# Optimization experiments

Measured on AMD Instinct MI355X. Metric: run time of the kernel, lower is better.

## Reference

```python
import jax, jax.numpy as jnp
import numpy as np

D_MODEL = 1024
D_STATE = 16
D_CONV = 4
EXPAND = 2
D_INNER = D_MODEL * EXPAND
B_SZ, L_SEQ = 4, 1024


def setup_inputs() -> dict:
    key = jax.random.key(0)
    ks = jax.random.split(key, 8)
    s = lambda fan_in: 1.0 / np.sqrt(fan_in)
    x = jax.random.normal(ks[0], (B_SZ, L_SEQ, D_MODEL), dtype=jnp.float32)
    in_proj_w = jax.random.uniform(ks[1], (2 * D_INNER, D_MODEL), jnp.float32, -s(D_MODEL), s(D_MODEL))
    conv_w = jax.random.uniform(ks[2], (D_INNER, 1, D_CONV), jnp.float32, -s(D_CONV), s(D_CONV))
    conv_b = jax.random.uniform(ks[3], (D_INNER,), jnp.float32, -s(D_CONV), s(D_CONV))
    x_proj_w = jax.random.uniform(ks[4], (2 * D_STATE + D_INNER, D_INNER), jnp.float32, -s(D_INNER), s(D_INNER))
    dt_proj_w = jax.random.uniform(ks[5], (D_INNER, D_INNER), jnp.float32, -s(D_INNER), s(D_INNER))
    dt_proj_b = jax.random.uniform(ks[6], (D_INNER,), jnp.float32, -1e-3, 1e-3)
    A = jnp.tile(jnp.arange(1, D_STATE + 1, dtype=jnp.float32), (D_INNER, 1))
    A_log = jnp.log(A)
    D_param = jnp.ones((D_INNER,), jnp.float32)
    out_proj_w = jax.random.uniform(ks[7], (D_MODEL, D_INNER), jnp.float32, -s(D_INNER), s(D_INNER))
    return {"x": x, "in_proj_w": in_proj_w, "conv_w": conv_w, "conv_b": conv_b,
            "x_proj_w": x_proj_w, "dt_proj_w": dt_proj_w, "dt_proj_b": dt_proj_b,
            "A_log": A_log, "D_param": D_param, "out_proj_w": out_proj_w}


def _selective_scan(x, delta, Bp, Cp, A_log, D_param):
    # x, delta: [B, L, D]; Bp, Cp: [B, L, N]
    A = -jnp.exp(A_log)                                   # [D, N]
    deltaA = jnp.exp(delta[..., None] * A)                # [B, L, D, N]
    deltaB_x = delta[..., None] * Bp[:, :, None, :] * x[..., None]  # [B, L, D, N]

    def step(h, inp):
        dA, dBx, Ct = inp                                 # [B,D,N], [B,D,N], [B,N]
        h = dA * h + dBx
        y = jnp.einsum('bn,bdn->bd', Ct, h)
        return h, y

    h0 = jnp.zeros((x.shape[0], x.shape[2], A.shape[1]), x.dtype)
    xs = (jnp.swapaxes(deltaA, 0, 1), jnp.swapaxes(deltaB_x, 0, 1), jnp.swapaxes(Cp, 0, 1))
    _, ys = jax.lax.scan(step, h0, xs)                    # ys: [L, B, D]
    return jnp.swapaxes(ys, 0, 1) + x * D_param


def reference(x, in_proj_w, conv_w, conv_b, x_proj_w, dt_proj_w, dt_proj_b, A_log, D_param, out_proj_w):
    B, L, _ = x.shape
    xz = x @ in_proj_w.T                                  # [B, L, 2*D_inner]
    xi, z = jnp.split(xz, 2, axis=-1)
    # causal depthwise conv (pad left K-1 == pad both & truncate to L)
    xc = jnp.swapaxes(xi, 1, 2)                           # [B, D_inner, L]
    xc = jax.lax.conv_general_dilated(xc, conv_w, window_strides=(1,),
                                      padding=[(D_CONV - 1, 0)],
                                      feature_group_count=D_INNER,
                                      dimension_numbers=('NCH', 'OIH', 'NCH'))
    xc = xc + conv_b[None, :, None]
    xi = jax.nn.silu(jnp.swapaxes(xc, 1, 2))              # [B, L, D_inner]
    deltaBC = xi @ x_proj_w.T
    delta, Bp, Cp = jnp.split(deltaBC, [D_INNER, D_INNER + D_STATE], axis=-1)
    delta = jax.nn.softplus(delta @ dt_proj_w.T + dt_proj_b)
    y = _selective_scan(xi, delta, Bp, Cp, A_log, D_param)
    return (y * jax.nn.silu(z)) @ out_proj_w.T
```

## Files before the change

### kernel.cpp

```cpp
#include <hip/hip_runtime.h>
#include <math.h>

#define B_SZ 4
#define L_SEQ 1024
#define D_MODEL 1024
#define D_INNER 2048
#define D_STATE 16
#define N_BC 2080
#define M_ROWS (B_SZ * L_SEQ)
#define CHUNK 32
#define NCH (L_SEQ / CHUNK)

typedef unsigned short u16;
typedef __bf16 bf16x8 __attribute__((ext_vector_type(8)));
typedef float f32x4 __attribute__((ext_vector_type(4)));

typedef const __attribute__((address_space(1))) unsigned short glb_u16;
typedef __attribute__((address_space(3))) unsigned short lds_u16;

__device__ __forceinline__ void gload_lds16(const u16* g, u16* l) {
    __builtin_amdgcn_global_load_lds((glb_u16*)g, (lds_u16*)l, 16, 0, 0);
}

__device__ __forceinline__ float bf2f(u16 u) {
    union { unsigned int i; float f; } v; v.i = ((unsigned int)u) << 16; return v.f;
}
__device__ __forceinline__ u16 f2bf(float f) {
    union { float f; unsigned int i; } v; v.f = f;
    return (u16)((v.i + 0x7FFFu + ((v.i >> 16) & 1u)) >> 16);
}
__device__ __forceinline__ float softplus_f(float v) {
    return fmaxf(v, 0.f) + log1pf(expf(-fabsf(v)));
}
__device__ __forceinline__ float silu_f(float v) {
    return v / (1.f + expf(-v));
}

__global__ __launch_bounds__(256) void cvt_bf16_k(const float* __restrict__ in,
                                                  u16* __restrict__ out, int n4) {
    int i = blockIdx.x * 256 + threadIdx.x;
    if (i >= n4) return;
    float4 v = *(const float4*)(in + (size_t)i * 4);
    ushort4 o;
    o.x = f2bf(v.x); o.y = f2bf(v.y); o.z = f2bf(v.z); o.w = f2bf(v.w);
    *(ushort4*)(out + (size_t)i * 4) = o;
}

template <int EPI>
__global__ __launch_bounds__(256, 2) void gemm_bf16(
    const u16* __restrict__ A, int lda,
    const u16* __restrict__ W, int ldw,
    int M, int N, int K, int ldc,
    const float* __restrict__ bias,
    float* __restrict__ Cf, u16* __restrict__ Cb, float* __restrict__ Caux)
{
    __shared__ __align__(16) u16 As[128 * 32];
    __shared__ __align__(16) u16 Ws[128 * 32];

    const int tid = threadIdx.x;
    const int lane = tid & 63;
    const int wave = tid >> 6;
    const int wr = wave >> 1;
    const int wc = wave & 1;
    const int bm = blockIdx.y * 128;
    const int bn = blockIdx.x * 128;
    const int l15 = lane & 15;
    const int lq = lane >> 4;

    const int lrow = lane >> 2;
    const int qoff = (((lane & 3) ^ ((lane >> 3) & 3))) * 8;
    const int rq = ((lq ^ ((l15 >> 1) & 3))) * 8;

    f32x4 acc[4][4];
#pragma unroll
    for (int m = 0; m < 4; ++m)
#pragma unroll
        for (int n = 0; n < 4; ++n) acc[m][n] = f32x4{0.f, 0.f, 0.f, 0.f};

    for (int k0 = 0; k0 < K; k0 += 32) {
#pragma unroll
        for (int i = 0; i < 2; ++i) {
            const int c = wave * 2 + i;
            const int row = c * 16 + lrow;
            gload_lds16(A + (size_t)(bm + row) * lda + k0 + qoff, &As[c * 512]);
            int wrow = bn + row; if (wrow >= N) wrow = N - 1;
            gload_lds16(W + (size_t)wrow * ldw + k0 + qoff, &Ws[c * 512]);
        }
        __syncthreads();

        bf16x8 af[4], bfr[4];
#pragma unroll
        for (int m = 0; m < 4; ++m) {
            int r = wr * 64 + m * 16 + l15;
            af[m] = *reinterpret_cast<const bf16x8*>(&As[r * 32 + rq]);
        }
#pragma unroll
        for (int n = 0; n < 4; ++n) {
            int r = wc * 64 + n * 16 + l15;
            bfr[n] = *reinterpret_cast<const bf16x8*>(&Ws[r * 32 + rq]);
        }
#pragma unroll
        for (int m = 0; m < 4; ++m)
#pragma unroll
            for (int n = 0; n < 4; ++n)
                acc[m][n] = __builtin_amdgcn_mfma_f32_16x16x32_bf16(af[m], bfr[n], acc[m][n], 0, 0, 0);
        __syncthreads();
    }

#pragma unroll
    for (int m = 0; m < 4; ++m) {
#pragma unroll
        for (int n = 0; n < 4; ++n) {
#pragma unroll
            for (int j = 0; j < 4; ++j) {
                int gr = bm + wr * 64 + m * 16 + lq * 4 + j;
                int gc = bn + wc * 64 + n * 16 + l15;
                float v = acc[m][n][j];
                if (EPI == 0) {
                    if (gc < N) Cf[(size_t)gr * ldc + gc] = v;
                } else if (EPI == 1) {
                    if (gc < N) Cf[(size_t)gr * ldc + gc] = softplus_f(v + bias[gc]);
                } else if (EPI == 2) {
                    if (gc < N) Cb[(size_t)gr * ldc + gc] = f2bf(v);
                } else {
                    if (gc < D_INNER) Cb[(size_t)gr * D_INNER + gc] = f2bf(v);
                    else if (gc < N_BC) Caux[(size_t)gr * 32 + (gc - D_INNER)] = v;
                }
            }
        }
    }
}

__global__ __launch_bounds__(256) void conv_silu_k(
    const u16* __restrict__ xz,
    const float* __restrict__ cw,
    const float* __restrict__ cb,
    u16* __restrict__ xc)
{
    int idx = blockIdx.x * 256 + threadIdx.x;
    if (idx >= M_ROWS * D_INNER) return;
    int d = idx & (D_INNER - 1);
    int m = idx >> 11;
    int l = m & (L_SEQ - 1);
    float4 w = *(const float4*)(cw + d * 4);
    const u16* base = xz + (size_t)m * (2 * D_INNER) + d;
    float acc = cb[d];
    acc = fmaf(bf2f(base[0]), w.w, acc);
    if (l >= 1) acc = fmaf(bf2f(base[-(2 * D_INNER)]), w.z, acc);
    if (l >= 2) acc = fmaf(bf2f(base[-2 * (2 * D_INNER)]), w.y, acc);
    if (l >= 3) acc = fmaf(bf2f(base[-3 * (2 * D_INNER)]), w.x, acc);
    xc[idx] = f2bf(silu_f(acc));
}

__global__ __launch_bounds__(256) void scan_pass1(
    const float* __restrict__ delta,
    const u16* __restrict__ xc,
    const float* __restrict__ BC,
    const float* __restrict__ A_log,
    float* __restrict__ hbuf,
    float* __restrict__ sumd)
{
    __shared__ float Bs[CHUNK][16];
    const int bid = blockIdx.x;
    const int c = bid & (NCH - 1);
    const int dblk = (bid >> 5) & 7;
    const int b = bid >> 8;
    const int tid = threadIdx.x;
    const int d = dblk * 256 + tid;
    const int row0 = b * L_SEQ + c * CHUNK;

    if (tid < CHUNK * 16) {
        int l = tid >> 4, n = tid & 15;
        Bs[l][n] = BC[(size_t)(row0 + l) * 32 + n];
    }
    __syncthreads();

    float Ac[16], h[16];
#pragma unroll
    for (int n = 0; n < 16; ++n) { Ac[n] = -__expf(A_log[d * 16 + n]); h[n] = 0.f; }
    float sd = 0.f;

    for (int l = 0; l < CHUNK; ++l) {
        size_t r = (size_t)(row0 + l);
        float dv = delta[r * D_INNER + d];
        float xv = bf2f(xc[r * D_INNER + d]);
        float t = dv * xv;
        sd += dv;
#pragma unroll
        for (int n = 0; n < 16; ++n) {
            float dA = __expf(dv * Ac[n]);
            h[n] = fmaf(dA, h[n], t * Bs[l][n]);
        }
    }
    size_t base = ((size_t)(b * NCH + c) * 16) * D_INNER + d;
#pragma unroll
    for (int n = 0; n < 16; ++n) hbuf[base + (size_t)n * D_INNER] = h[n];
    sumd[(size_t)(b * NCH + c) * D_INNER + d] = sd;
}

__global__ __launch_bounds__(256) void scan_pass2(
    const float* __restrict__ A_log,
    const float* __restrict__ sumd,
    float* __restrict__ hbuf)
{
    const int bid = blockIdx.x;
    const int dblk = bid & 7;
    const int n = (bid >> 3) & 15;
    const int b = bid >> 7;
    const int d = dblk * 256 + threadIdx.x;
    const float Ac = -__expf(A_log[d * 16 + n]);
    float carry = 0.f;
    for (int c = 0; c < NCH; ++c) {
        float sd = sumd[(size_t)(b * NCH + c) * D_INNER + d];
        size_t idx = ((size_t)(b * NCH + c) * 16 + n) * D_INNER + d;
        float tmp = hbuf[idx];
        hbuf[idx] = carry;
        carry = fmaf(__expf(Ac * sd), carry, tmp);
    }
}

__global__ __launch_bounds__(256) void scan_pass3(
    const float* __restrict__ delta,
    const u16* __restrict__ xc,
    const float* __restrict__ BC,
    const u16* __restrict__ xz,
    const float* __restrict__ A_log,
    const float* __restrict__ Dp,
    const float* __restrict__ hbuf,
    u16* __restrict__ yg)
{
    __shared__ float BCs[CHUNK][32];
    const int bid = blockIdx.x;
    const int c = bid & (NCH - 1);
    const int dblk = (bid >> 5) & 7;
    const int b = bid >> 8;
    const int tid = threadIdx.x;
    const int d = dblk * 256 + tid;
    const int row0 = b * L_SEQ + c * CHUNK;

#pragma unroll
    for (int i = 0; i < (CHUNK * 32) / 256; ++i) {
        int e = tid + i * 256;
        int l = e >> 5, j = e & 31;
        BCs[l][j] = BC[(size_t)(row0 + l) * 32 + j];
    }
    __syncthreads();

    float Ac[16], h[16];
    size_t base = ((size_t)(b * NCH + c) * 16) * D_INNER + d;
#pragma unroll
    for (int n = 0; n < 16; ++n) {
        Ac[n] = -__expf(A_log[d * 16 + n]);
        h[n] = hbuf[base + (size_t)n * D_INNER];
    }
    const float Dv = Dp[d];

    for (int l = 0; l < CHUNK; ++l) {
        size_t r = (size_t)(row0 + l);
        float dv = delta[r * D_INNER + d];
        float xv = bf2f(xc[r * D_INNER + d]);
        float t = dv * xv;
        float y = xv * Dv;
#pragma unroll
        for (int n = 0; n < 16; ++n) {
            float dA = __expf(dv * Ac[n]);
            h[n] = fmaf(dA, h[n], t * BCs[l][n]);
            y = fmaf(BCs[l][16 + n], h[n], y);
        }
        float zv = bf2f(xz[r * (2 * D_INNER) + D_INNER + d]);
        yg[r * D_INNER + d] = f2bf(y * silu_f(zv));
    }
}

extern "C" void kernel_launch(void* const* d_in, const int* in_sizes, int n_in,
                              void* d_out, int out_size, void* d_ws, size_t ws_size,
                              hipStream_t stream)
{
    const float* x          = (const float*)d_in[0];
    const float* in_proj_w  = (const float*)d_in[1];
    const float* conv_w     = (const float*)d_in[2];
    const float* conv_b     = (const float*)d_in[3];
    const float* x_proj_w   = (const float*)d_in[4];
    const float* dt_proj_w  = (const float*)d_in[5];
    const float* dt_proj_b  = (const float*)d_in[6];
    const float* A_log      = (const float*)d_in[7];
    const float* D_param    = (const float*)d_in[8];
    const float* out_proj_w = (const float*)d_in[9];
    float* out = (float*)d_out;

    char* p = (char*)d_ws;
    u16* x_bf  = (u16*)p;  p += (size_t)M_ROWS * D_MODEL * 2;
    u16* w1_bf = (u16*)p;  p += (size_t)2 * D_INNER * D_MODEL * 2;
    u16* w3_bf = (u16*)p;  p += (size_t)N_BC * D_INNER * 2;
    u16* w4_bf = (u16*)p;  p += (size_t)D_INNER * D_INNER * 2;
    u16* w6_bf = (u16*)p;  p += (size_t)D_MODEL * D_INNER * 2;
    u16* xz_bf = (u16*)p;  p += (size_t)M_ROWS * 2 * D_INNER * 2;
    u16* xc_bf = (u16*)p;  p += (size_t)M_ROWS * D_INNER * 2;
    u16* dt_bf = (u16*)p;  p += (size_t)M_ROWS * D_INNER * 2;
    float* BC  = (float*)p; p += (size_t)M_ROWS * 32 * 4;
    float* delta = (float*)p; p += (size_t)M_ROWS * D_INNER * 4;
    u16* yg_bf = (u16*)p;
    float* hbuf = (float*)dt_bf;
    float* sumd = (float*)x_bf;

    dim3 blk(256);
    auto cvt = [&](const float* src, u16* dst, size_t n) {
        int n4 = (int)(n / 4);
        cvt_bf16_k<<<dim3((n4 + 255) / 256), blk, 0, stream>>>(src, dst, n4);
    };
    cvt(x,          x_bf,  (size_t)M_ROWS * D_MODEL);
    cvt(in_proj_w,  w1_bf, (size_t)2 * D_INNER * D_MODEL);
    cvt(x_proj_w,   w3_bf, (size_t)N_BC * D_INNER);
    cvt(dt_proj_w,  w4_bf, (size_t)D_INNER * D_INNER);
    cvt(out_proj_w, w6_bf, (size_t)D_MODEL * D_INNER);

    gemm_bf16<2><<<dim3(32, 32), blk, 0, stream>>>(
        x_bf, D_MODEL, w1_bf, D_MODEL, M_ROWS, 2 * D_INNER, D_MODEL, 2 * D_INNER,
        nullptr, nullptr, xz_bf, nullptr);

    conv_silu_k<<<dim3((M_ROWS * D_INNER) / 256), blk, 0, stream>>>(
        xz_bf, conv_w, conv_b, xc_bf);

    gemm_bf16<3><<<dim3(17, 32), blk, 0, stream>>>(
        xc_bf, D_INNER, w3_bf, D_INNER, M_ROWS, N_BC, D_INNER, 0,
        nullptr, nullptr, dt_bf, BC);

    gemm_bf16<1><<<dim3(16, 32), blk, 0, stream>>>(
        dt_bf, D_INNER, w4_bf, D_INNER, M_ROWS, D_INNER, D_INNER, D_INNER,
        dt_proj_b, delta, nullptr, nullptr);

    scan_pass1<<<dim3(B_SZ * 8 * NCH), blk, 0, stream>>>(
        delta, xc_bf, BC, A_log, hbuf, sumd);
    scan_pass2<<<dim3(B_SZ * 16 * 8), blk, 0, stream>>>(
        A_log, sumd, hbuf);
    scan_pass3<<<dim3(B_SZ * 8 * NCH), blk, 0, stream>>>(
        delta, xc_bf, BC, xz_bf, A_log, D_param, hbuf, yg_bf);

    gemm_bf16<0><<<dim3(8, 32), blk, 0, stream>>>(
        yg_bf, D_INNER, w6_bf, D_INNER, M_ROWS, D_MODEL, D_INNER, D_MODEL,
        nullptr, out, nullptr, nullptr);
}
```

Baseline: 342.5 us.

## Double-buffer GEMM LDS tiles and fuse bf16 conversion launches

The bf16 GEMM now uses two LDS buffers. It issues the async global-to-LDS load of the next K tile before computing on the current one, which removes one barrier per iteration and overlaps memory with MFMA. The five separate fp32-to-bf16 conversion kernels are merged into one launch that writes into the contiguous workspace region. In exchange, LDS use per block doubles, which may lower occupancy, and correctness depends on the barrier ordering of the async loads.

```diff
diff --git a/kernel.cpp b/kernel.cpp
--- a/kernel.cpp
+++ b/kernel.cpp
@@ -36,14 +36,25 @@
     return v / (1.f + expf(-v));
 }
 
-__global__ __launch_bounds__(256) void cvt_bf16_k(const float* __restrict__ in,
-                                                  u16* __restrict__ out, int n4) {
+__global__ __launch_bounds__(256) void cvt5_bf16_k(
+    const float* __restrict__ s0, const float* __restrict__ s1,
+    const float* __restrict__ s2, const float* __restrict__ s3,
+    const float* __restrict__ s4,
+    u16* __restrict__ dst,
+    int e0, int e1, int e2, int e3, int e4)
+{
     int i = blockIdx.x * 256 + threadIdx.x;
-    if (i >= n4) return;
-    float4 v = *(const float4*)(in + (size_t)i * 4);
+    if (i >= e4) return;
+    const float* src; int base;
+    if (i < e0)      { src = s0; base = 0;  }
+    else if (i < e1) { src = s1; base = e0; }
+    else if (i < e2) { src = s2; base = e1; }
+    else if (i < e3) { src = s3; base = e2; }
+    else             { src = s4; base = e3; }
+    float4 v = *(const float4*)(src + (size_t)(i - base) * 4);
     ushort4 o;
     o.x = f2bf(v.x); o.y = f2bf(v.y); o.z = f2bf(v.z); o.w = f2bf(v.w);
-    *(ushort4*)(out + (size_t)i * 4) = o;
+    *(ushort4*)(dst + (size_t)i * 4) = o;
 }
 
 template <int EPI>
@@ -54,8 +65,8 @@
     const float* __restrict__ bias,
     float* __restrict__ Cf, u16* __restrict__ Cb, float* __restrict__ Caux)
 {
-    __shared__ __align__(16) u16 As[128 * 32];
-    __shared__ __align__(16) u16 Ws[128 * 32];
+    __shared__ __align__(16) u16 As[2][128 * 32];
+    __shared__ __align__(16) u16 Ws[2][128 * 32];
 
     const int tid = threadIdx.x;
     const int lane = tid & 63;
@@ -77,34 +88,44 @@
 #pragma unroll
         for (int n = 0; n < 4; ++n) acc[m][n] = f32x4{0.f, 0.f, 0.f, 0.f};
 
-    for (int k0 = 0; k0 < K; k0 += 32) {
+    auto stage = [&](int buf, int k0) {
 #pragma unroll
         for (int i = 0; i < 2; ++i) {
             const int c = wave * 2 + i;
             const int row = c * 16 + lrow;
-            gload_lds16(A + (size_t)(bm + row) * lda + k0 + qoff, &As[c * 512]);
+            gload_lds16(A + (size_t)(bm + row) * lda + k0 + qoff, &As[buf][c * 512]);
             int wrow = bn + row; if (wrow >= N) wrow = N - 1;
-            gload_lds16(W + (size_t)wrow * ldw + k0 + qoff, &Ws[c * 512]);
-        }
-        __syncthreads();
+            gload_lds16(W + (size_t)wrow * ldw + k0 + qoff, &Ws[buf][c * 512]);
+        }
+    };
+
+    const int nt = K >> 5;
+    stage(0, 0);
+    __syncthreads();
+
+    int cur = 0;
+    for (int t = 0; t < nt; ++t) {
+        if (t + 1 < nt) stage(cur ^ 1, (t + 1) << 5);
 
         bf16x8 af[4], bfr[4];
 #pragma unroll
         for (int m = 0; m < 4; ++m) {
             int r = wr * 64 + m * 16 + l15;
-            af[m] = *reinterpret_cast<const bf16x8*>(&As[r * 32 + rq]);
+            af[m] = *reinterpret_cast<const bf16x8*>(&As[cur][r * 32 + rq]);
         }
 #pragma unroll
         for (int n = 0; n < 4; ++n) {
             int r = wc * 64 + n * 16 + l15;
-            bfr[n] = *reinterpret_cast<const bf16x8*>(&Ws[r * 32 + rq]);
+            bfr[n] = *reinterpret_cast<const bf16x8*>(&Ws[cur][r * 32 + rq]);
         }
 #pragma unroll
         for (int m = 0; m < 4; ++m)
 #pragma unroll
             for (int n = 0; n < 4; ++n)
                 acc[m][n] = __builtin_amdgcn_mfma_f32_16x16x32_bf16(af[m], bfr[n], acc[m][n], 0, 0, 0);
-        __syncthreads();
+
+        if (t + 1 < nt) __syncthreads();
+        cur ^= 1;
     }
 
 #pragma unroll
@@ -304,15 +325,18 @@
     float* sumd = (float*)x_bf;
 
     dim3 blk(256);
-    auto cvt = [&](const float* src, u16* dst, size_t n) {
-        int n4 = (int)(n / 4);
-        cvt_bf16_k<<<dim3((n4 + 255) / 256), blk, 0, stream>>>(src, dst, n4);
-    };
-    cvt(x,          x_bf,  (size_t)M_ROWS * D_MODEL);
-    cvt(in_proj_w,  w1_bf, (size_t)2 * D_INNER * D_MODEL);
-    cvt(x_proj_w,   w3_bf, (size_t)N_BC * D_INNER);
-    cvt(dt_proj_w,  w4_bf, (size_t)D_INNER * D_INNER);
-    cvt(out_proj_w, w6_bf, (size_t)D_MODEL * D_INNER);
+
+    {
+        const int n0 = (M_ROWS * D_MODEL) / 4;
+        const int n1 = (2 * D_INNER * D_MODEL) / 4;
+        const int n2 = (N_BC * D_INNER) / 4;
+        const int n3 = (D_INNER * D_INNER) / 4;
+        const int n4 = (D_MODEL * D_INNER) / 4;
+        const int e0 = n0, e1 = e0 + n1, e2 = e1 + n2, e3 = e2 + n3, e4 = e3 + n4;
+        cvt5_bf16_k<<<dim3((e4 + 255) / 256), blk, 0, stream>>>(
+            x, in_proj_w, x_proj_w, dt_proj_w, out_proj_w,
+            x_bf, e0, e1, e2, e3, e4);
+    }
 
     gemm_bf16<2><<<dim3(32, 32), blk, 0, stream>>>(
         x_bf, D_MODEL, w1_bf, D_MODEL, M_ROWS, 2 * D_INNER, D_MODEL, 2 * D_INNER,
```

Result: no change. 344.2 us (+0.5%).
